# Performance work log

Hardware: AMD Instinct MI355X
Metric: run time of the kernel (lower is better)

Reference implementation:

```python
import jax, jax.numpy as jnp
import numpy as np

EPS = 1e-3  # Keras BatchNormalization default epsilon
B = 4096
TX = 32
SUB = 13


def setup_inputs() -> dict:
    key = jax.random.key(0)
    ks = jax.random.split(key, 24)
    f32 = jnp.float32
    n = lambda k, s: jax.random.normal(k, s, dtype=f32)
    u = lambda k, s: jax.random.uniform(k, s, dtype=f32)
    W_SCALE = jnp.float32(0.05)  # keras truncated_normal default stddev
    inp = {
        'V1': n(ks[0], (B, TX, SUB, 2)),
        'V2': n(ks[1], (B, TX, SUB, 2)),
        'W1': n(ks[2], (2, 64, 1024)) * W_SCALE,
        'b1': n(ks[3], (2, 1024)) * W_SCALE,
        'g1': u(ks[4], (2, 1024)) + jnp.float32(0.5),
        'be1': n(ks[5], (2, 1024)) * jnp.float32(0.1),
        'm1': n(ks[6], (2, 1024)) * jnp.float32(0.1),
        'v1': u(ks[7], (2, 1024)) + jnp.float32(0.5),
        'W2': n(ks[8], (2, 1024, 512)) * W_SCALE,
        'b2': n(ks[9], (2, 512)) * W_SCALE,
        'g2': u(ks[10], (2, 512)) + jnp.float32(0.5),
        'be2': n(ks[11], (2, 512)) * jnp.float32(0.1),
        'm2': n(ks[12], (2, 512)) * jnp.float32(0.1),
        'v2': u(ks[13], (2, 512)) + jnp.float32(0.5),
        'W3': n(ks[14], (2, 512, 512)) * W_SCALE,
        'b3': n(ks[15], (2, 512)) * W_SCALE,
        'g3': u(ks[16], (2, 512)) + jnp.float32(0.5),
        'be3': n(ks[17], (2, 512)) * jnp.float32(0.1),
        'm3': n(ks[18], (2, 512)) * jnp.float32(0.1),
        'v3': u(ks[19], (2, 512)) + jnp.float32(0.5),
        'W4': n(ks[20], (2, 512, 64)) * W_SCALE,
        'b4': n(ks[21], (2, 64)) * W_SCALE,
    }
    return inp


def _dense_bn_relu(x, W, b, g, be, m, v):
    # Dense(activation='relu') followed by BatchNormalization (inference mode),
    # batched over the tower dim t in {real, imag}.
    h = jax.nn.relu(jnp.einsum('tbi,tio->tbo', x, W) + b[:, None, :])
    return (h - m[:, None, :]) * (g[:, None, :] * jax.lax.rsqrt(v[:, None, :] + EPS)) + be[:, None, :]


def reference(V1, V2, W1, b1, g1, be1, m1, v1, W2, b2, g2, be2, m2, v2,
              W3, b3, g3, be3, m3, v3, W4, b4):
    # Per-UE input normalization over (tx, real/imag) per subband
    def norm_in(V):
        return V / jnp.sqrt(jnp.sum(V * V, axis=(1, 3), keepdims=True))

    inp = jnp.concatenate([norm_in(V1), norm_in(V2)], axis=1)  # (B, 2*TX, SUB, 2)
    b = inp.shape[0]
    # Vectorize the 13-subband python loop: (B, 64, SUB, 2) -> (2 towers, B*SUB, 64)
    x = jnp.transpose(inp, (3, 0, 2, 1)).reshape(2, b * SUB, 2 * TX)

    h = _dense_bn_relu(x, W1, b1, g1, be1, m1, v1)
    h = _dense_bn_relu(h, W2, b2, g2, be2, m2, v2)
    h = _dense_bn_relu(h, W3, b3, g3, be3, m3, v3)
    z = jnp.einsum('tbi,tio->tbo', h, W4) + b4[:, None, :]  # (2, B*SUB, 64)

    V_r = z[0].reshape(b, SUB, TX, 2)                   # linear head (real tower)
    V_i = jax.nn.sigmoid(z[1]).reshape(b, SUB, TX, 2)   # sigmoid head (imag tower)

    # Per-subband, per-UE joint L2 normalization over the 32 tx antennas
    nrm = jnp.sqrt(jnp.sum(V_r * V_r + V_i * V_i, axis=2, keepdims=True))  # (B, SUB, 1, 2)
    V_r = V_r / nrm
    V_i = V_i / nrm

    # C2R + transpose per UE: (B, SUB, TX) complex -> (B, TX, SUB, 2) real
    def per_ue(u):
        return jnp.transpose(jnp.stack([V_r[..., u], V_i[..., u]], axis=-1), (0, 2, 1, 3))

    mix_V = jnp.concatenate([per_ue(0), per_ue(1)], axis=1)  # (B, 2*TX, SUB, 2)
    return mix_V
```

## Files before the change

### kernel.cpp

```cpp
#include <hip/hip_runtime.h>
#include <hip/hip_bf16.h>

typedef __attribute__((ext_vector_type(8))) short bf16x8;
typedef __attribute__((ext_vector_type(4))) float f32x4;

#define GLOAD16(gsrc, ldst)                                                    \
  __builtin_amdgcn_global_load_lds(                                            \
      (const __attribute__((address_space(1))) unsigned int*)(const void*)(gsrc), \
      (__attribute__((address_space(3))) unsigned int*)(void*)(ldst), 16, 0, 0)

static constexpr int    MROWS = 53248;
static constexpr size_t M64   = (size_t)MROWS * 64;

__global__ void transpose_w(const float* __restrict__ W, __hip_bfloat16* __restrict__ Wt,
                            int K, int N) {
  int total = 2 * K * N;
  int idx = blockIdx.x * 256 + threadIdx.x;
  if (idx >= total) return;
  int t   = idx / (K * N);
  int rem = idx - t * K * N;
  int n   = rem / K;
  int k   = rem - n * K;
  Wt[idx] = __float2bfloat16(W[(size_t)t * K * N + (size_t)k * N + n]);
}

__global__ void bn_prep(const float* __restrict__ g, const float* __restrict__ be,
                        const float* __restrict__ m, const float* __restrict__ v,
                        float* __restrict__ s, float* __restrict__ o, int n) {
  int i = blockIdx.x * 256 + threadIdx.x;
  if (i < n) {
    float sc = g[i] * rsqrtf(v[i] + 1e-3f);
    s[i] = sc;
    o[i] = be[i] - m[i] * sc;
  }
}

__global__ __launch_bounds__(256) void input_norm(const float* __restrict__ V1,
                                                  const float* __restrict__ V2,
                                                  __hip_bfloat16* __restrict__ x) {
  __shared__ float lv[1664];
  __shared__ float inv_s[26];
  const int b = blockIdx.x, tid = threadIdx.x;
  for (int idx = tid; idx < 1664; idx += 256)
    lv[idx] = (idx < 832) ? V1[(size_t)b * 832 + idx] : V2[(size_t)b * 832 + idx - 832];
  __syncthreads();
  if (tid < 26) {
    int ue = tid / 13, s = tid - ue * 13;
    const float* base = &lv[ue * 832 + s * 2];
    float sum = 0.f;
#pragma unroll
    for (int tx = 0; tx < 32; ++tx) {
      float a = base[tx * 26], c = base[tx * 26 + 1];
      sum += a * a + c * c;
    }
    inv_s[tid] = rsqrtf(sum);
  }
  __syncthreads();
  for (int idx = tid; idx < 1664; idx += 256) {
    int t = idx / 832, rem = idx - t * 832;
    int s = rem >> 6, c = rem & 63;
    int ue = c >> 5, tx = c & 31;
    float val = lv[ue * 832 + tx * 26 + s * 2 + t] * inv_s[ue * 13 + s];
    x[(size_t)t * M64 + (size_t)(b * 13 + s) * 64 + c] = __float2bfloat16(val);
  }
}

template <int N, int K, int BN, int ACT>
__global__ __launch_bounds__(256) void gemm_bn(const __hip_bfloat16* __restrict__ A,
                                               size_t strideA, int aRow0,
                                               const __hip_bfloat16* __restrict__ Wt,
                                               const float* __restrict__ bias,
                                               const float* __restrict__ sc,
                                               const float* __restrict__ ofs,
                                               __hip_bfloat16* __restrict__ Y,
                                               float* __restrict__ Z,
                                               size_t strideO) {
  constexpr int BM = 128, BK = 64;
  constexpr int MI = 4, NI = BN / 32;
  constexpr int AI = (BM * BK) / (256 * 8);
  constexpr int BI = (BN * BK) / (256 * 8);
  __shared__ __align__(16) __hip_bfloat16 lsA[BM * BK];
  __shared__ __align__(16) __hip_bfloat16 lsB[BN * BK];

  const int t = blockIdx.z;
  const int m0 = blockIdx.y * BM;
  const int n0 = blockIdx.x * BN;
  const int tid = threadIdx.x;
  const int lane = tid & 63, wave = tid >> 6;
  const int wr = wave >> 1, wc = wave & 1;
  const int l15 = lane & 15, lhi = lane >> 4;

  const __hip_bfloat16* Ab = A + (size_t)t * strideA;
  const __hip_bfloat16* Wb = Wt + (size_t)t * N * K;

  f32x4 acc[MI][NI];
#pragma unroll
  for (int i = 0; i < MI; ++i)
#pragma unroll
    for (int j = 0; j < NI; ++j) acc[i][j] = (f32x4){0.f, 0.f, 0.f, 0.f};

  for (int k0 = 0; k0 < K; k0 += BK) {
#pragma unroll
    for (int c = 0; c < AI; ++c) {
      int e = (c * 256 + tid) * 8;
      GLOAD16(&Ab[(size_t)(aRow0 + m0 + (e >> 6)) * K + k0 + (e & 63)],
              &lsA[(c * 256 + wave * 64) * 8]);
    }
#pragma unroll
    for (int c = 0; c < BI; ++c) {
      int e = (c * 256 + tid) * 8;
      GLOAD16(&Wb[(size_t)(n0 + (e >> 6)) * K + k0 + (e & 63)],
              &lsB[(c * 256 + wave * 64) * 8]);
    }
    __syncthreads();
#pragma unroll
    for (int kk = 0; kk < 2; ++kk) {
      bf16x8 af[MI], bfr[NI];
#pragma unroll
      for (int i = 0; i < MI; ++i)
        af[i] = *(const bf16x8*)&lsA[(wr * 64 + i * 16 + l15) * BK + kk * 32 + lhi * 8];
#pragma unroll
      for (int j = 0; j < NI; ++j)
        bfr[j] = *(const bf16x8*)&lsB[(wc * (BN / 2) + j * 16 + l15) * BK + kk * 32 + lhi * 8];
#pragma unroll
      for (int i = 0; i < MI; ++i)
#pragma unroll
        for (int j = 0; j < NI; ++j)
          acc[i][j] = __builtin_amdgcn_mfma_f32_16x16x32_bf16(af[i], bfr[j], acc[i][j], 0, 0, 0);
    }
    __syncthreads();
  }

  const int gcb = n0 + wc * (BN / 2) + l15;
  float bi[NI], si[NI], oi[NI];
#pragma unroll
  for (int j = 0; j < NI; ++j) {
    int gc = gcb + j * 16;
    bi[j] = bias[t * N + gc];
    if constexpr (ACT) {
      si[j] = sc[t * N + gc];
      oi[j] = ofs[t * N + gc];
    }
  }
#pragma unroll
  for (int i = 0; i < MI; ++i) {
    int grow = m0 + wr * 64 + i * 16 + lhi * 4;
#pragma unroll
    for (int j = 0; j < NI; ++j) {
      int gc = gcb + j * 16;
#pragma unroll
      for (int r = 0; r < 4; ++r) {
        float val = acc[i][j][r] + bi[j];
        if constexpr (ACT) {
          val = fmaxf(val, 0.f) * si[j] + oi[j];
          Y[(size_t)t * strideO + (size_t)(grow + r) * N + gc] = __float2bfloat16(val);
        } else {
          Z[(size_t)t * strideO + (size_t)(grow + r) * N + gc] = val;
        }
      }
    }
  }
}

__global__ __launch_bounds__(256) void postproc(const float* __restrict__ Z,
                                                size_t zstride, int row0,
                                                float* __restrict__ out) {
  const int zrow = blockIdx.x * 4 + (threadIdx.x >> 6);
  const int o = threadIdx.x & 63;
  float zr = Z[(size_t)zrow * 64 + o];
  float zl = Z[zstride + (size_t)zrow * 64 + o];
  float vi = 1.f / (1.f + expf(-zl));
  float p = zr * zr + vi * vi;
  p += __shfl_xor(p, 2);
  p += __shfl_xor(p, 4);
  p += __shfl_xor(p, 8);
  p += __shfl_xor(p, 16);
  p += __shfl_xor(p, 32);
  float inv = rsqrtf(p);
  int grow = row0 + zrow;
  int bb = grow / 13, s = grow - bb * 13;
  int tx = o >> 1, ue = o & 1;
  size_t base = (((size_t)bb * 64 + ue * 32 + tx) * 13 + s) * 2;
  out[base]     = zr * inv;
  out[base + 1] = vi * inv;
}

extern "C" void kernel_launch(void* const* d_in, const int* in_sizes, int n_in,
                              void* d_out, int out_size, void* d_ws, size_t ws_size,
                              hipStream_t stream) {
  const float* V1 = (const float*)d_in[0];
  const float* V2 = (const float*)d_in[1];
  const float* W1 = (const float*)d_in[2];
  const float* b1 = (const float*)d_in[3];
  const float* g1 = (const float*)d_in[4];
  const float* be1 = (const float*)d_in[5];
  const float* m1 = (const float*)d_in[6];
  const float* v1 = (const float*)d_in[7];
  const float* W2 = (const float*)d_in[8];
  const float* b2 = (const float*)d_in[9];
  const float* g2 = (const float*)d_in[10];
  const float* be2 = (const float*)d_in[11];
  const float* m2 = (const float*)d_in[12];
  const float* v2 = (const float*)d_in[13];
  const float* W3 = (const float*)d_in[14];
  const float* b3 = (const float*)d_in[15];
  const float* g3 = (const float*)d_in[16];
  const float* be3 = (const float*)d_in[17];
  const float* m3 = (const float*)d_in[18];
  const float* v3 = (const float*)d_in[19];
  const float* W4 = (const float*)d_in[20];
  const float* b4 = (const float*)d_in[21];
  float* out = (float*)d_out;

  char* ws = (char*)d_ws;
  constexpr size_t OFF_WT1 = 0;
  constexpr size_t OFF_WT2 = OFF_WT1 + 262144;
  constexpr size_t OFF_WT3 = OFF_WT2 + 2097152;
  constexpr size_t OFF_WT4 = OFF_WT3 + 1048576;
  constexpr size_t OFF_S1  = OFF_WT4 + 131072;
  constexpr size_t OFF_O1  = OFF_S1 + 8192;
  constexpr size_t OFF_S2  = OFF_O1 + 8192;
  constexpr size_t OFF_O2  = OFF_S2 + 4096;
  constexpr size_t OFF_S3  = OFF_O2 + 4096;
  constexpr size_t OFF_O3  = OFF_S3 + 4096;
  constexpr size_t OFF_X   = OFF_O3 + 4096;
  constexpr size_t FIXED_END = OFF_X + 13631488;

  __hip_bfloat16* wt1 = (__hip_bfloat16*)(ws + OFF_WT1);
  __hip_bfloat16* wt2 = (__hip_bfloat16*)(ws + OFF_WT2);
  __hip_bfloat16* wt3 = (__hip_bfloat16*)(ws + OFF_WT3);
  __hip_bfloat16* wt4 = (__hip_bfloat16*)(ws + OFF_WT4);
  float* s1 = (float*)(ws + OFF_S1);
  float* o1 = (float*)(ws + OFF_O1);
  float* s2 = (float*)(ws + OFF_S2);
  float* o2 = (float*)(ws + OFF_O2);
  float* s3 = (float*)(ws + OFF_S3);
  float* o3 = (float*)(ws + OFF_O3);
  __hip_bfloat16* xb = (__hip_bfloat16*)(ws + OFF_X);

  constexpr int TOT_BLOCKS = 416;
  size_t avail = (ws_size > FIXED_END) ? (ws_size - FIXED_END) : 0;
  long sb = (long)(avail / ((size_t)8704 * 128));
  int seg_blocks = (sb < 1) ? 1 : (sb > TOT_BLOCKS ? TOT_BLOCKS : (int)sb);
  const int seg_rows = seg_blocks * 128;
  const size_t H1E = (size_t)seg_rows * 1024;
  const size_t H2E = (size_t)seg_rows * 512;
  const size_t ZE  = (size_t)seg_rows * 64;
  const size_t OFF_H1 = FIXED_END;
  const size_t OFF_H2 = OFF_H1 + 2 * H1E * 2;
  const size_t OFF_H3 = OFF_H2 + 2 * H2E * 2;
  const size_t OFF_Z  = OFF_H3 + 2 * H2E * 2;
  __hip_bfloat16* h1 = (__hip_bfloat16*)(ws + OFF_H1);
  __hip_bfloat16* h2 = (__hip_bfloat16*)(ws + OFF_H2);
  __hip_bfloat16* h3 = (__hip_bfloat16*)(ws + OFF_H3);
  float*          zb = (float*)(ws + OFF_Z);

  transpose_w<<<(2 * 64 * 1024 + 255) / 256, 256, 0, stream>>>(W1, wt1, 64, 1024);
  transpose_w<<<(2 * 1024 * 512 + 255) / 256, 256, 0, stream>>>(W2, wt2, 1024, 512);
  transpose_w<<<(2 * 512 * 512 + 255) / 256, 256, 0, stream>>>(W3, wt3, 512, 512);
  transpose_w<<<(2 * 512 * 64 + 255) / 256, 256, 0, stream>>>(W4, wt4, 512, 64);
  bn_prep<<<8, 256, 0, stream>>>(g1, be1, m1, v1, s1, o1, 2048);
  bn_prep<<<4, 256, 0, stream>>>(g2, be2, m2, v2, s2, o2, 1024);
  bn_prep<<<4, 256, 0, stream>>>(g3, be3, m3, v3, s3, o3, 1024);

  input_norm<<<4096, 256, 0, stream>>>(V1, V2, xb);

  for (int bl0 = 0; bl0 < TOT_BLOCKS; bl0 += seg_blocks) {
    int nb = (TOT_BLOCKS - bl0 < seg_blocks) ? (TOT_BLOCKS - bl0) : seg_blocks;
    int r0 = bl0 * 128;
    gemm_bn<1024, 64, 128, 1><<<dim3(8, nb, 2), 256, 0, stream>>>(
        xb, M64, r0, wt1, b1, s1, o1, h1, nullptr, H1E);
    gemm_bn<512, 1024, 128, 1><<<dim3(4, nb, 2), 256, 0, stream>>>(
        h1, H1E, 0, wt2, b2, s2, o2, h2, nullptr, H2E);
    gemm_bn<512, 512, 128, 1><<<dim3(4, nb, 2), 256, 0, stream>>>(
        h2, H2E, 0, wt3, b3, s3, o3, h3, nullptr, H2E);
    gemm_bn<64, 512, 64, 0><<<dim3(1, nb, 2), 256, 0, stream>>>(
        h3, H2E, 0, wt4, b4, nullptr, nullptr, nullptr, zb, ZE);
    postproc<<<nb * 32, 256, 0, stream>>>(zb, ZE, r0, out);
  }

  (void)in_sizes; (void)n_in; (void)out_size;
}
```

Baseline: 558.1 us.

## Load GEMM fragments directly from global memory and remap workgroups across XCDs

The GEMM kernel no longer stages A and W tiles through LDS with global_load_lds and barriers. Each wave now reads its bf16x8 MFMA fragments straight from global memory. The grid is flattened to 1D, and the block index is remapped so that consecutive logical tiles land on the same XCD, which should improve L2 locality. This removes LDS traffic and synchronisation but loses intra-block sharing of tiles, so every wave re-fetches A and B rows through the caches, and the per-lane 16-byte strided loads may coalesce poorly.

```diff
diff --git a/kernel.cpp b/kernel.cpp
--- a/kernel.cpp
+++ b/kernel.cpp
@@ -3,11 +3,6 @@
 
 typedef __attribute__((ext_vector_type(8))) short bf16x8;
 typedef __attribute__((ext_vector_type(4))) float f32x4;
-
-#define GLOAD16(gsrc, ldst)                                                    \
-  __builtin_amdgcn_global_load_lds(                                            \
-      (const __attribute__((address_space(1))) unsigned int*)(const void*)(gsrc), \
-      (__attribute__((address_space(3))) unsigned int*)(void*)(ldst), 16, 0, 0)
 
 static constexpr int    MROWS = 53248;
 static constexpr size_t M64   = (size_t)MROWS * 64;
@@ -66,32 +61,35 @@
 }
 
 template <int N, int K, int BN, int ACT>
-__global__ __launch_bounds__(256) void gemm_bn(const __hip_bfloat16* __restrict__ A,
-                                               size_t strideA, int aRow0,
-                                               const __hip_bfloat16* __restrict__ Wt,
-                                               const float* __restrict__ bias,
-                                               const float* __restrict__ sc,
-                                               const float* __restrict__ ofs,
-                                               __hip_bfloat16* __restrict__ Y,
-                                               float* __restrict__ Z,
-                                               size_t strideO) {
-  constexpr int BM = 128, BK = 64;
+__global__ __launch_bounds__(256) void gemm_direct(const __hip_bfloat16* __restrict__ A,
+                                                   size_t strideA, int aRow0,
+                                                   const __hip_bfloat16* __restrict__ Wt,
+                                                   const float* __restrict__ bias,
+                                                   const float* __restrict__ sc,
+                                                   const float* __restrict__ ofs,
+                                                   __hip_bfloat16* __restrict__ Y,
+                                                   float* __restrict__ Z,
+                                                   size_t strideO, int nby) {
+  constexpr int GX = N / BN;
   constexpr int MI = 4, NI = BN / 32;
-  constexpr int AI = (BM * BK) / (256 * 8);
-  constexpr int BI = (BN * BK) / (256 * 8);
-  __shared__ __align__(16) __hip_bfloat16 lsA[BM * BK];
-  __shared__ __align__(16) __hip_bfloat16 lsB[BN * BK];
-
-  const int t = blockIdx.z;
-  const int m0 = blockIdx.y * BM;
-  const int n0 = blockIdx.x * BN;
-  const int tid = threadIdx.x;
-  const int lane = tid & 63, wave = tid >> 6;
+
+  const int nwg = GX * nby * 2;
+  const int L   = blockIdx.x;
+  const int q = nwg >> 3, r = nwg & 7;
+  const int xcd = L & 7, idx = L >> 3;
+  const int wg = (xcd < r ? xcd * (q + 1) : r * (q + 1) + (xcd - r) * q) + idx;
+  const int t   = wg / (GX * nby);
+  const int rem = wg - t * (GX * nby);
+  const int by  = rem / GX;
+  const int bx  = rem - by * GX;
+  const int m0 = by * 128, n0 = bx * BN;
+
+  const int lane = threadIdx.x & 63, wave = threadIdx.x >> 6;
   const int wr = wave >> 1, wc = wave & 1;
   const int l15 = lane & 15, lhi = lane >> 4;
 
-  const __hip_bfloat16* Ab = A + (size_t)t * strideA;
-  const __hip_bfloat16* Wb = Wt + (size_t)t * N * K;
+  const __hip_bfloat16* Ab = A + (size_t)t * strideA + (size_t)(aRow0 + m0) * K;
+  const __hip_bfloat16* Wb = Wt + (size_t)t * N * K + (size_t)n0 * K;
 
   f32x4 acc[MI][NI];
 #pragma unroll
@@ -99,36 +97,24 @@
 #pragma unroll
     for (int j = 0; j < NI; ++j) acc[i][j] = (f32x4){0.f, 0.f, 0.f, 0.f};
 
-  for (int k0 = 0; k0 < K; k0 += BK) {
-#pragma unroll
-    for (int c = 0; c < AI; ++c) {
-      int e = (c * 256 + tid) * 8;
-      GLOAD16(&Ab[(size_t)(aRow0 + m0 + (e >> 6)) * K + k0 + (e & 63)],
-              &lsA[(c * 256 + wave * 64) * 8]);
-    }
-#pragma unroll
-    for (int c = 0; c < BI; ++c) {
-      int e = (c * 256 + tid) * 8;
-      GLOAD16(&Wb[(size_t)(n0 + (e >> 6)) * K + k0 + (e & 63)],
-              &lsB[(c * 256 + wave * 64) * 8]);
-    }
-    __syncthreads();
+#pragma unroll 2
+  for (int k0 = 0; k0 < K; k0 += 64) {
 #pragma unroll
     for (int kk = 0; kk < 2; ++kk) {
+      const int ko = k0 + kk * 32 + lhi * 8;
       bf16x8 af[MI], bfr[NI];
 #pragma unroll
       for (int i = 0; i < MI; ++i)
-        af[i] = *(const bf16x8*)&lsA[(wr * 64 + i * 16 + l15) * BK + kk * 32 + lhi * 8];
+        af[i] = *(const bf16x8*)&Ab[(size_t)(wr * 64 + i * 16 + l15) * K + ko];
 #pragma unroll
       for (int j = 0; j < NI; ++j)
-        bfr[j] = *(const bf16x8*)&lsB[(wc * (BN / 2) + j * 16 + l15) * BK + kk * 32 + lhi * 8];
+        bfr[j] = *(const bf16x8*)&Wb[(size_t)(wc * (BN / 2) + j * 16 + l15) * K + ko];
 #pragma unroll
       for (int i = 0; i < MI; ++i)
 #pragma unroll
         for (int j = 0; j < NI; ++j)
           acc[i][j] = __builtin_amdgcn_mfma_f32_16x16x32_bf16(af[i], bfr[j], acc[i][j], 0, 0, 0);
     }
-    __syncthreads();
   }
 
   const int gcb = n0 + wc * (BN / 2) + l15;
@@ -149,13 +135,13 @@
     for (int j = 0; j < NI; ++j) {
       int gc = gcb + j * 16;
 #pragma unroll
-      for (int r = 0; r < 4; ++r) {
-        float val = acc[i][j][r] + bi[j];
+      for (int rr = 0; rr < 4; ++rr) {
+        float val = acc[i][j][rr] + bi[j];
         if constexpr (ACT) {
           val = fmaxf(val, 0.f) * si[j] + oi[j];
-          Y[(size_t)t * strideO + (size_t)(grow + r) * N + gc] = __float2bfloat16(val);
+          Y[(size_t)t * strideO + (size_t)(grow + rr) * N + gc] = __float2bfloat16(val);
         } else {
-          Z[(size_t)t * strideO + (size_t)(grow + r) * N + gc] = val;
+          Z[(size_t)t * strideO + (size_t)(grow + rr) * N + gc] = val;
         }
       }
     }
@@ -268,14 +254,14 @@
   for (int bl0 = 0; bl0 < TOT_BLOCKS; bl0 += seg_blocks) {
     int nb = (TOT_BLOCKS - bl0 < seg_blocks) ? (TOT_BLOCKS - bl0) : seg_blocks;
     int r0 = bl0 * 128;
-    gemm_bn<1024, 64, 128, 1><<<dim3(8, nb, 2), 256, 0, stream>>>(
-        xb, M64, r0, wt1, b1, s1, o1, h1, nullptr, H1E);
-    gemm_bn<512, 1024, 128, 1><<<dim3(4, nb, 2), 256, 0, stream>>>(
-        h1, H1E, 0, wt2, b2, s2, o2, h2, nullptr, H2E);
-    gemm_bn<512, 512, 128, 1><<<dim3(4, nb, 2), 256, 0, stream>>>(
-        h2, H2E, 0, wt3, b3, s3, o3, h3, nullptr, H2E);
-    gemm_bn<64, 512, 64, 0><<<dim3(1, nb, 2), 256, 0, stream>>>(
-        h3, H2E, 0, wt4, b4, nullptr, nullptr, nullptr, zb, ZE);
+    gemm_direct<1024, 64, 128, 1><<<8 * nb * 2, 256, 0, stream>>>(
+        xb, M64, r0, wt1, b1, s1, o1, h1, nullptr, H1E, nb);
+    gemm_direct<512, 1024, 128, 1><<<4 * nb * 2, 256, 0, stream>>>(
+        h1, H1E, 0, wt2, b2, s2, o2, h2, nullptr, H2E, nb);
+    gemm_direct<512, 512, 128, 1><<<4 * nb * 2, 256, 0, stream>>>(
+        h2, H2E, 0, wt3, b3, s3, o3, h3, nullptr, H2E, nb);
+    gemm_direct<64, 512, 64, 0><<<1 * nb * 2, 256, 0, stream>>>(
+        h3, H2E, 0, wt4, b4, nullptr, nullptr, nullptr, zb, ZE, nb);
     postproc<<<nb * 32, 256, 0, stream>>>(zb, ZE, r0, out);
   }
 
```

Result: slower. 990.9 us (+77.5%).
